# Kernel tuning notes

Hardware: AMD Instinct MI355X
Metric: run time of the kernel (lower is better)

Reference implementation:

```python
import jax, jax.numpy as jnp
import numpy as np

NUM_HEADS = 2
LN_EPS = 1e-5
NEG_MASK = -1e9


def setup_inputs() -> dict:
    key = jax.random.key(0)
    ks = jax.random.split(key, 8)
    B, C, T, N = 8, 64, 32, 400
    H, D = NUM_HEADS, C // NUM_HEADS
    s = 1.0 / np.sqrt(C)
    return {
        "x": jax.random.normal(ks[0], (B, C, T, N), dtype=jnp.float32),
        "Wq": jax.random.normal(ks[1], (C, C), dtype=jnp.float32) * s,
        "Wk": jax.random.normal(ks[2], (C, C), dtype=jnp.float32) * s,
        "Wv": jax.random.normal(ks[3], (C, C), dtype=jnp.float32) * s,
        "a_src": jax.random.normal(ks[4], (H, D), dtype=jnp.float32) * 0.1,
        "a_dst": jax.random.normal(ks[5], (H, D), dtype=jnp.float32) * 0.1,
        "ln_gamma": jnp.ones((C,), dtype=jnp.float32),
        "ln_beta": jnp.zeros((C,), dtype=jnp.float32),
        "gso": jax.random.randint(ks[6], (N, N), 0, 2, dtype=jnp.int32),
    }


def reference(x, Wq, Wk, Wv, a_src, a_dst, ln_gamma, ln_beta, gso):
    B, C, T, N = x.shape
    H = NUM_HEADS
    D = C // H
    # (B,C,T,N) -> (B*T, N, C)
    xr = jnp.transpose(x, (0, 2, 3, 1)).reshape(B * T, N, C)
    # torch Linear: y = x @ W.T; then split heads -> (BT, N, H, D)
    Q = (xr @ Wq.T).reshape(B * T, N, H, D)
    K = (xr @ Wk.T).reshape(B * T, N, H, D)
    V = (xr @ Wv.T).reshape(B * T, N, H, D)
    # GAT additive scores per head
    s_src = jnp.einsum("bnhd,hd->bnh", Q, a_src)  # (BT, N, H)
    s_dst = jnp.einsum("bnhd,hd->bnh", K, a_dst)  # (BT, N, H)
    scores = s_src[:, :, None, :] + s_dst[:, None, :, :]  # (BT, i, j, H)
    scores = jax.nn.leaky_relu(scores, negative_slope=0.2)
    mask = jnp.where(gso == 0, jnp.float32(NEG_MASK), 0.0)  # (N, N)
    scores = scores + mask[None, :, :, None]
    attn = jax.nn.softmax(scores, axis=2)  # softmax over dst j; dropout = identity (eval)
    out = jnp.einsum("bijh,bjhd->bihd", attn, V).reshape(B * T, N, C)
    # LayerNorm over channel dim
    mu = jnp.mean(out, axis=-1, keepdims=True)
    var = jnp.var(out, axis=-1, keepdims=True)
    out = (out - mu) * jax.lax.rsqrt(var + LN_EPS) * ln_gamma + ln_beta
    # (BT, N, C) -> (B, C, T, N)
    return jnp.transpose(out.reshape(B, T, N, C), (0, 3, 1, 2))
```

## Files before the change

kernel.cpp:

```cpp
#include <hip/hip_runtime.h>
#include <hip/hip_bf16.h>

typedef __attribute__((ext_vector_type(8))) short bf16x8;
typedef __attribute__((ext_vector_type(4))) float f32x4;
typedef __attribute__((ext_vector_type(2))) float f32x2;
typedef __attribute__((ext_vector_type(4))) int i32x4;
typedef __attribute__((ext_vector_type(4))) unsigned int u32x4;

#define B_   8
#define C_   64
#define T_   32
#define N_   400
#define BT_  256
#define NKT_ 13
#define L2E_ 1.4426950408889634f
#define C2_  (-13.849872392533959f)
#define SH12_ (-17.312340490667560f)

#if __has_builtin(__builtin_amdgcn_exp2f)
#define EXP2F(x) __builtin_amdgcn_exp2f(x)
#else
#define EXP2F(x) __expf((x) * 0.6931471805599453f)
#endif

__global__ __launch_bounds__(256) void gat_prep(
    const int* __restrict__ gso, unsigned int* __restrict__ mb)
{
  int idx = blockIdx.x*256 + threadIdx.x;
  if (idx < N_*16) {
    int i = idx >> 4, kw = idx & 15;
    unsigned int bits = 0;
    if (kw < 13) {
      int j0 = kw * 32;
      #pragma unroll
      for (int bb = 0; bb < 32; ++bb) {
        int j = j0 + bb;
        if (j < N_ && gso[i*N_ + j] != 0) bits |= (1u << bb);
      }
    }
    mb[idx] = bits;
  }
}

__global__ __launch_bounds__(1024) void gat_fused(
    const float* __restrict__ x, const float* __restrict__ Wq,
    const float* __restrict__ Wk, const float* __restrict__ Wv,
    const float* __restrict__ a_src, const float* __restrict__ a_dst,
    const float* __restrict__ gamma, const float* __restrict__ beta,
    const unsigned int* __restrict__ mb, float* __restrict__ out)
{
  __shared__ __align__(16) __hip_bfloat16 Vt[64][416];
  __shared__ __align__(16) char scratch[70656];
  __shared__ __align__(16) float sd_s[2][416];
  __shared__ __align__(16) float si_s[2][400];
  __shared__ float wqk_s[4][64];
  __shared__ float g_s[64], b_s[64];

  unsigned int (*xs)[208] = (unsigned int(*)[208])scratch;
  float (*wv_s)[68] = (float(*)[68])(scratch + 53248);
  float (*ob)[68] = (float(*)[68])scratch;

  const int tid = threadIdx.x;
  const int bt = blockIdx.x;
  const int b = bt >> 5, t = bt & 31;

  if (tid < 256) {
    int ww = tid >> 6, c = tid & 63, h = ww >> 1;
    const float* W = (ww & 1) ? Wk : Wq;
    const float* a = (ww & 1) ? a_dst : a_src;
    float s = 0.f;
    #pragma unroll
    for (int d = 0; d < 32; ++d) s += W[(h*32 + d)*C_ + c] * a[h*32 + d];
    wqk_s[ww][c] = s;
  } else if (tid < 320) {
    g_s[tid - 256] = gamma[tid - 256];
  } else if (tid < 384) {
    b_s[tid - 320] = beta[tid - 320];
  }
  #pragma unroll
  for (int it = 0; it < 4; ++it) {
    int idx = it*1024 + tid;
    int o = idx >> 6, c = idx & 63;
    wv_s[c][o] = Wv[o*C_ + c];
  }
  #pragma unroll
  for (int it = 0; it < 16; ++it) {
    int idx = it*1024 + tid;
    int c = idx >> 8, pr = idx & 255;
    if (pr < 208) {
      int n = pr*2;
      const float* xrow = x + ((size_t)(b*C_ + c)*T_ + t)*N_;
      float x0 = (n   < N_) ? xrow[n]   : 0.f;
      float x1 = (n+1 < N_) ? xrow[n+1] : 0.f;
      union { __hip_bfloat16 h2[2]; unsigned int u; } pk;
      pk.h2[0] = __float2bfloat16(x0);
      pk.h2[1] = __float2bfloat16(x1);
      xs[c][pr] = pk.u;
    }
  }
  __syncthreads();

  {
    const int pr = tid >> 2, ww = tid & 3;
    if (pr < 208) {
      f32x2 acc[16];
      #pragma unroll
      for (int k = 0; k < 16; ++k) acc[k] = (f32x2){0.f, 0.f};
      f32x2 sacc = {0.f, 0.f};
      #pragma unroll 4
      for (int c = 0; c < 64; ++c) {
        unsigned int xu = xs[c][pr];
        f32x2 xv;
        xv.x = __uint_as_float(xu << 16);
        xv.y = __uint_as_float(xu & 0xffff0000u);
        const f32x4* wr = (const f32x4*)&wv_s[c][ww*16];
        f32x4 w0 = wr[0], w1 = wr[1], w2 = wr[2], w3 = wr[3];
        #pragma unroll
        for (int k = 0; k < 4; ++k) acc[k]      = xv * w0[k] + acc[k];
        #pragma unroll
        for (int k = 0; k < 4; ++k) acc[4 + k]  = xv * w1[k] + acc[4 + k];
        #pragma unroll
        for (int k = 0; k < 4; ++k) acc[8 + k]  = xv * w2[k] + acc[8 + k];
        #pragma unroll
        for (int k = 0; k < 4; ++k) acc[12 + k] = xv * w3[k] + acc[12 + k];
        sacc = xv * wqk_s[ww][c] + sacc;
      }
      const int n = pr*2, hw = ww >> 1;
      if (ww & 1) {
        sd_s[hw][n]   = sacc.x * L2E_;
        sd_s[hw][n+1] = sacc.y * L2E_;
      } else {
        if (n   < N_) si_s[hw][n]   = fmaf(sacc.x, L2E_, SH12_);
        if (n+1 < N_) si_s[hw][n+1] = fmaf(sacc.y, L2E_, SH12_);
      }
      #pragma unroll
      for (int k = 0; k < 16; ++k) {
        int o = ww*16 + k;
        union { __hip_bfloat16 h2[2]; unsigned int u; } pk;
        pk.h2[0] = __float2bfloat16(acc[k].x);
        pk.h2[1] = __float2bfloat16(acc[k].y);
        *(unsigned int*)&Vt[o][n] = pk.u;
      }
    }
  }
  __syncthreads();

  const int lane = tid & 63, wave = tid >> 6;
  const int hh = wave & 1, itile = wave >> 1;
  const int rowA = lane & 15, quad = lane >> 4;

  bf16x8 ones;
  #pragma unroll
  for (int k = 0; k < 8; ++k) ones[k] = (short)0x3F80;

  for (int r0 = 0; r0 < N_; r0 += 128) {
    const int ibase = r0 + itile*16;
    if (ibase < N_) {
      const int irow = ibase + rowA;
      const float si1 = si_s[hh][irow];
      const u32x4* mp = (const u32x4*)(mb + irow*16);
      u32x4 mw0 = mp[0], mw1 = mp[1], mw2 = mp[2];
      unsigned int mw12 = mb[irow*16 + 12];
      const float* sdp = sd_s[hh] + quad*8;
      const __hip_bfloat16* v0p = &Vt[hh*32 + rowA][quad*8];
      const __hip_bfloat16* v1p = v0p + 16*416;

      f32x4 d0 = {0,0,0,0}, d1 = {0,0,0,0}, d2 = {0,0,0,0};
      #pragma unroll
      for (int kt = 0; kt < NKT_; ++kt) {
        unsigned int mword = (kt < 4) ? mw0[kt] : (kt < 8) ? mw1[kt-4]
                           : (kt < 12) ? mw2[kt-8] : mw12;
        unsigned int mbyte = (mword >> (quad*8)) & 0xffu;
        f32x4 s0 = *(const f32x4*)(sdp + kt*32);
        f32x4 s1 = *(const f32x4*)(sdp + kt*32 + 4);
        bf16x8 vb0 = *(const bf16x8*)(v0p + kt*32);
        bf16x8 vb1 = *(const bf16x8*)(v1p + kt*32);
        int em[8];
        #pragma unroll
        for (int jj = 0; jj < 8; ++jj) {
          float sd = (jj < 4) ? s0[jj] : s1[jj-4];
          float t1 = si1 + sd;
          float t2 = fmaf(0.2f, t1, C2_);
          float v  = fmaxf(t1, t2);
          float e  = EXP2F(v);
          int msk = ((int)(mbyte << (31 - jj))) >> 31;
          em[jj] = __float_as_int(e) & msk;
        }
        union { i32x4 i; bf16x8 v; } af;
        af.i.x = (int)__builtin_amdgcn_perm((unsigned)em[1], (unsigned)em[0], 0x07060302u);
        af.i.y = (int)__builtin_amdgcn_perm((unsigned)em[3], (unsigned)em[2], 0x07060302u);
        af.i.z = (int)__builtin_amdgcn_perm((unsigned)em[5], (unsigned)em[4], 0x07060302u);
        af.i.w = (int)__builtin_amdgcn_perm((unsigned)em[7], (unsigned)em[6], 0x07060302u);
        d0 = __builtin_amdgcn_mfma_f32_16x16x32_bf16(af.v, vb0, d0, 0, 0, 0);
        d1 = __builtin_amdgcn_mfma_f32_16x16x32_bf16(af.v, vb1, d1, 0, 0, 0);
        d2 = __builtin_amdgcn_mfma_f32_16x16x32_bf16(af.v, ones, d2, 0, 0, 0);
      }
      #pragma unroll
      for (int r = 0; r < 4; ++r) {
        float li = 1.0f / d2[r];
        int rl = itile*16 + quad*4 + r;
        ob[rl][hh*32 + rowA]      = d0[r] * li;
        ob[rl][hh*32 + 16 + rowA] = d1[r] * li;
      }
    }
    __syncthreads();

    {
      int rl = tid >> 3, cgi = tid & 7;
      int n = r0 + rl;
      if (n < N_) {
        float u[8]; float s = 0.f;
        #pragma unroll
        for (int k = 0; k < 8; ++k) { u[k] = ob[rl][cgi*8 + k]; s += u[k]; }
        s += __shfl_xor(s,1); s += __shfl_xor(s,2); s += __shfl_xor(s,4);
        float mu = s * (1.f/64.f);
        float q = 0.f;
        #pragma unroll
        for (int k = 0; k < 8; ++k) { float dv = u[k]-mu; q = fmaf(dv,dv,q); }
        q += __shfl_xor(q,1); q += __shfl_xor(q,2); q += __shfl_xor(q,4);
        float rstd = rsqrtf(q*(1.f/64.f) + 1e-5f);
        #pragma unroll
        for (int k = 0; k < 8; ++k)
          ob[rl][cgi*8 + k] = (u[k]-mu)*rstd*g_s[cgi*8 + k] + b_s[cgi*8 + k];
      }
    }
    __syncthreads();

    #pragma unroll
    for (int it = 0; it < 8; ++it) {
      int idx = it*1024 + tid;
      int c = idx >> 7, nn = idx & 127;
      int n = r0 + nn;
      if (n < N_) out[((size_t)(b*C_ + c)*T_ + t)*N_ + n] = ob[nn][c];
    }
    __syncthreads();
  }
}

extern "C" void kernel_launch(void* const* d_in, const int* in_sizes, int n_in,
                              void* d_out, int out_size, void* d_ws, size_t ws_size,
                              hipStream_t stream) {
  (void)in_sizes; (void)n_in; (void)out_size; (void)ws_size;
  const float* x     = (const float*)d_in[0];
  const float* Wq    = (const float*)d_in[1];
  const float* Wk    = (const float*)d_in[2];
  const float* Wv    = (const float*)d_in[3];
  const float* a_src = (const float*)d_in[4];
  const float* a_dst = (const float*)d_in[5];
  const float* gamma = (const float*)d_in[6];
  const float* beta  = (const float*)d_in[7];
  const int*   gso   = (const int*)d_in[8];
  float* out = (float*)d_out;

  unsigned int* mb = (unsigned int*)d_ws;

  gat_prep<<<26, 256, 0, stream>>>(gso, mb);
  gat_fused<<<BT_, 1024, 0, stream>>>(x, Wq, Wk, Wv, a_src, a_dst,
                                      gamma, beta, mb, out);
}
```

Before: 139.8 us.

## Compute V projection and score vectors with bf16 MFMA instead of scalar FMAs

Replaces the scalar per-thread V projection and the score dot products (staged x in LDS, fp32 FMA loops) with 16x16x32 bf16 MFMA tiles. Each wave loads x straight from global memory into B fragments and multiplies against a bf16 Wv matrix that carries the folded Wq·a_src and Wk·a_dst rows as extra output rows. This removes the LDS staging of x and most of the VALU work in the projection phase. In exchange the global x loads are strided per lane and less coalesced, the score weights are rounded to bf16, only 25 of 16 waves' tiles keep the work uneven, and the LDS layout changes (row padding 424 and 72, dedicated ob buffer).

```diff
diff --git a/kernel.cpp b/kernel.cpp
--- a/kernel.cpp
+++ b/kernel.cpp
@@ -3,7 +3,6 @@
 
 typedef __attribute__((ext_vector_type(8))) short bf16x8;
 typedef __attribute__((ext_vector_type(4))) float f32x4;
-typedef __attribute__((ext_vector_type(2))) float f32x2;
 typedef __attribute__((ext_vector_type(4))) int i32x4;
 typedef __attribute__((ext_vector_type(4))) unsigned int u32x4;
 
@@ -13,6 +12,9 @@
 #define N_   400
 #define BT_  256
 #define NKT_ 13
+#define CN_  12800
+#define VROW 424
+#define WROW 72
 #define L2E_ 1.4426950408889634f
 #define C2_  (-13.849872392533959f)
 #define SH12_ (-17.312340490667560f)
@@ -49,21 +51,25 @@
     const float* __restrict__ gamma, const float* __restrict__ beta,
     const unsigned int* __restrict__ mb, float* __restrict__ out)
 {
-  __shared__ __align__(16) __hip_bfloat16 Vt[64][416];
-  __shared__ __align__(16) char scratch[70656];
+  __shared__ __align__(16) __hip_bfloat16 Vt[64][VROW];
+  __shared__ __align__(16) __hip_bfloat16 wvb[80][WROW];
   __shared__ __align__(16) float sd_s[2][416];
   __shared__ __align__(16) float si_s[2][400];
-  __shared__ float wqk_s[4][64];
+  __shared__ __align__(16) float ob[128][68];
   __shared__ float g_s[64], b_s[64];
-
-  unsigned int (*xs)[208] = (unsigned int(*)[208])scratch;
-  float (*wv_s)[68] = (float(*)[68])(scratch + 53248);
-  float (*ob)[68] = (float(*)[68])scratch;
 
   const int tid = threadIdx.x;
   const int bt = blockIdx.x;
   const int b = bt >> 5, t = bt & 31;
-
+  const int lane = tid & 63, wave = tid >> 6;
+  const int col = lane & 15, quad = lane >> 4;
+
+  #pragma unroll
+  for (int it = 0; it < 4; ++it) {
+    int idx = it*1024 + tid;
+    int o = idx >> 6, c = idx & 63;
+    wvb[o][c] = __float2bfloat16(Wv[o*C_ + c]);
+  }
   if (tid < 256) {
     int ww = tid >> 6, c = tid & 63, h = ww >> 1;
     const float* W = (ww & 1) ? Wk : Wq;
@@ -71,83 +77,65 @@
     float s = 0.f;
     #pragma unroll
     for (int d = 0; d < 32; ++d) s += W[(h*32 + d)*C_ + c] * a[h*32 + d];
-    wqk_s[ww][c] = s;
+    wvb[64 + ww][c] = __float2bfloat16(s * L2E_);
   } else if (tid < 320) {
     g_s[tid - 256] = gamma[tid - 256];
   } else if (tid < 384) {
     b_s[tid - 320] = beta[tid - 320];
-  }
-  #pragma unroll
-  for (int it = 0; it < 4; ++it) {
-    int idx = it*1024 + tid;
-    int o = idx >> 6, c = idx & 63;
-    wv_s[c][o] = Wv[o*C_ + c];
-  }
-  #pragma unroll
-  for (int it = 0; it < 16; ++it) {
-    int idx = it*1024 + tid;
-    int c = idx >> 8, pr = idx & 255;
-    if (pr < 208) {
-      int n = pr*2;
-      const float* xrow = x + ((size_t)(b*C_ + c)*T_ + t)*N_;
-      float x0 = (n   < N_) ? xrow[n]   : 0.f;
-      float x1 = (n+1 < N_) ? xrow[n+1] : 0.f;
-      union { __hip_bfloat16 h2[2]; unsigned int u; } pk;
-      pk.h2[0] = __float2bfloat16(x0);
-      pk.h2[1] = __float2bfloat16(x1);
-      xs[c][pr] = pk.u;
-    }
-  }
+  } else if (tid < 416) {
+    int tt = tid - 384;
+    sd_s[tt >> 4][400 + (tt & 15)] = 0.f;
+  }
+  for (int idx = tid; idx < 12*WROW; idx += 1024)
+    wvb[68 + idx/WROW][idx % WROW] = __float2bfloat16(0.f);
+  for (int idx = tid; idx < 64*24; idx += 1024)
+    Vt[idx/24][400 + idx%24] = __float2bfloat16(0.f);
   __syncthreads();
 
   {
-    const int pr = tid >> 2, ww = tid & 3;
-    if (pr < 208) {
-      f32x2 acc[16];
-      #pragma unroll
-      for (int k = 0; k < 16; ++k) acc[k] = (f32x2){0.f, 0.f};
-      f32x2 sacc = {0.f, 0.f};
-      #pragma unroll 4
-      for (int c = 0; c < 64; ++c) {
-        unsigned int xu = xs[c][pr];
-        f32x2 xv;
-        xv.x = __uint_as_float(xu << 16);
-        xv.y = __uint_as_float(xu & 0xffff0000u);
-        const f32x4* wr = (const f32x4*)&wv_s[c][ww*16];
-        f32x4 w0 = wr[0], w1 = wr[1], w2 = wr[2], w3 = wr[3];
-        #pragma unroll
-        for (int k = 0; k < 4; ++k) acc[k]      = xv * w0[k] + acc[k];
-        #pragma unroll
-        for (int k = 0; k < 4; ++k) acc[4 + k]  = xv * w1[k] + acc[4 + k];
-        #pragma unroll
-        for (int k = 0; k < 4; ++k) acc[8 + k]  = xv * w2[k] + acc[8 + k];
-        #pragma unroll
-        for (int k = 0; k < 4; ++k) acc[12 + k] = xv * w3[k] + acc[12 + k];
-        sacc = xv * wqk_s[ww][c] + sacc;
-      }
-      const int n = pr*2, hw = ww >> 1;
-      if (ww & 1) {
-        sd_s[hw][n]   = sacc.x * L2E_;
-        sd_s[hw][n+1] = sacc.y * L2E_;
-      } else {
-        if (n   < N_) si_s[hw][n]   = fmaf(sacc.x, L2E_, SH12_);
-        if (n+1 < N_) si_s[hw][n+1] = fmaf(sacc.y, L2E_, SH12_);
-      }
-      #pragma unroll
-      for (int k = 0; k < 16; ++k) {
-        int o = ww*16 + k;
-        union { __hip_bfloat16 h2[2]; unsigned int u; } pk;
-        pk.h2[0] = __float2bfloat16(acc[k].x);
-        pk.h2[1] = __float2bfloat16(acc[k].y);
-        *(unsigned int*)&Vt[o][n] = pk.u;
+    const float* xbase = x + ((size_t)b*C_*T_ + t)*N_;
+    for (int nt = wave; nt < 25; nt += 16) {
+      const int n0 = nt*16;
+      bf16x8 bfrag[2];
+      #pragma unroll
+      for (int kt = 0; kt < 2; ++kt) {
+        const float* xc = xbase + (size_t)(kt*32 + quad*8)*CN_ + n0 + col;
+        union { short s[8]; bf16x8 v; } pk;
+        #pragma unroll
+        for (int j = 0; j < 8; ++j) {
+          union { __hip_bfloat16 h; short s; } cv;
+          cv.h = __float2bfloat16(xc[(size_t)j*CN_]);
+          pk.s[j] = cv.s;
+        }
+        bfrag[kt] = pk.v;
+      }
+      #pragma unroll
+      for (int ot = 0; ot < 5; ++ot) {
+        f32x4 acc = {0.f, 0.f, 0.f, 0.f};
+        #pragma unroll
+        for (int kt = 0; kt < 2; ++kt) {
+          bf16x8 afr = *(const bf16x8*)&wvb[ot*16 + col][kt*32 + quad*8];
+          acc = __builtin_amdgcn_mfma_f32_16x16x32_bf16(afr, bfrag[kt], acc, 0, 0, 0);
+        }
+        if (ot < 4) {
+          #pragma unroll
+          for (int r = 0; r < 4; ++r)
+            Vt[ot*16 + quad*4 + r][n0 + col] = __float2bfloat16(acc[r]);
+        } else if (quad == 0) {
+          #pragma unroll
+          for (int r = 0; r < 4; ++r) {
+            int h = r >> 1;
+            if (r & 1) sd_s[h][n0 + col] = acc[r];
+            else       si_s[h][n0 + col] = acc[r] + SH12_;
+          }
+        }
       }
     }
   }
   __syncthreads();
 
-  const int lane = tid & 63, wave = tid >> 6;
   const int hh = wave & 1, itile = wave >> 1;
-  const int rowA = lane & 15, quad = lane >> 4;
+  const int rowA = col;
 
   bf16x8 ones;
   #pragma unroll
@@ -163,7 +151,7 @@
       unsigned int mw12 = mb[irow*16 + 12];
       const float* sdp = sd_s[hh] + quad*8;
       const __hip_bfloat16* v0p = &Vt[hh*32 + rowA][quad*8];
-      const __hip_bfloat16* v1p = v0p + 16*416;
+      const __hip_bfloat16* v1p = v0p + 16*VROW;
 
       f32x4 d0 = {0,0,0,0}, d1 = {0,0,0,0}, d2 = {0,0,0,0};
       #pragma unroll
```

Measured after the change: 122.4 us. -12.4%, faster.
